# Kernel optimization log

Measured on AMD Instinct MI355X. Metric: run time of the kernel, lower is better.

The kernel has to match this reference:

```python
import jax, jax.numpy as jnp
import numpy as np
from jax import lax

EPS = 1e-5
K = 80000 // 16  # sample_pixels // 16 selected regions per image


def _conv(x, w):
    return lax.conv_general_dilated(x, w, (1, 1), 'VALID',
                                    dimension_numbers=('NHWC', 'HWIO', 'NHWC'))


def _bn(x, g, b, m, v):
    # Keras BatchNormalization in inference mode
    return (x - m) * (g * lax.rsqrt(v + EPS)) + b


def _crop(x, bi, iy, ix, size, pad):
    # tf.image.crop_and_resize with 'nearest' and integer-aligned boxes of span
    # (size+2*pad) reduces to a zero-padded window gather (out-of-bounds -> 0).
    S = size + 2 * pad
    xp = jnp.pad(x, ((0, 0), (pad, pad), (pad, pad), (0, 0)))
    rows = iy[:, None] * size + jnp.arange(S)[None, :]  # padded coords (offset -pad+pad)
    cols = ix[:, None] * size + jnp.arange(S)[None, :]
    return xp[bi[:, None, None], rows[:, :, None], cols[:, None, :], :]  # [N,S,S,C]


def _replace(x, y, bi, iy, ix):
    # scatter 4x4 patches y [N,4,4,C] back into x [B,H,W,C] at block (iy,ix)
    B, H, W, C = x.shape
    x6 = x.reshape(B, H // 4, 4, W // 4, 4, C).transpose(0, 1, 3, 2, 4, 5)
    x6 = x6.at[bi, iy, ix].set(y)
    return x6.transpose(0, 1, 3, 2, 4, 5).reshape(B, H, W, C)


def _forward(src, bgr, pha, fgr, err, hid,
             w1, g1, b1, m1, v1, w2, g2, b2, m2, v2,
             w3, g3, b3, m3, v3, w4, b4):
    B, Hf, Wf = src.shape[:3]
    Hh, Wh, Hq, Wq = Hf // 2, Wf // 2, Hf // 4, Wf // 4
    src_bgr = jnp.concatenate([src, bgr], axis=-1)

    # err already at quarter resolution -> tf bilinear resize is identity
    top_idx = lax.top_k(err[..., 0].reshape(B, -1), K)[1]  # [B,K]
    ref = jnp.zeros((B, Hq * Wq), err.dtype).at[jnp.arange(B)[:, None], top_idx].set(1.0)
    ref = ref.reshape(B, Hq, Wq, 1) * (err > 0).astype(err.dtype)

    bi = jnp.repeat(jnp.arange(B), K)          # [N] patch batch index, N = B*K
    iy = (top_idx // Wq).reshape(-1)
    ix = (top_idx % Wq).reshape(-1)

    x = jnp.concatenate([hid, pha, fgr], axis=-1)  # [B,Hq,Wq,36]
    x = jax.image.resize(x, (B, Hh, Wh, x.shape[-1]), 'bilinear')
    xp = _crop(x, bi, iy, ix, 2, 3)                # [N,8,8,36]
    yh = jax.image.resize(src_bgr, (B, Hh, Wh, 6), 'bilinear')
    yp = _crop(yh, bi, iy, ix, 2, 3)               # [N,8,8,6]

    t = jax.nn.relu(_bn(_conv(jnp.concatenate([xp, yp], -1), w1), g1, b1, m1, v1))  # [N,6,6,24]
    t = jax.nn.relu(_bn(_conv(t, w2), g2, b2, m2, v2))                              # [N,4,4,16]
    t = jax.image.resize(t, (t.shape[0], 8, 8, t.shape[-1]), 'nearest')
    y2 = _crop(src_bgr, bi, iy, ix, 4, 2)                                           # [N,8,8,6]
    t = jax.nn.relu(_bn(_conv(jnp.concatenate([t, y2], -1), w3), g3, b3, m3, v3))   # [N,6,6,12]
    t = _conv(t, w4) + b4                                                            # [N,4,4,4]

    pha_f = jax.image.resize(pha, (B, Hf, Wf, 1), 'bilinear')
    fgr_f = jax.image.resize(fgr, (B, Hf, Wf, 3), 'bilinear')
    pha_f = _replace(pha_f, t[..., :1], bi, iy, ix)
    fgr_f = _replace(fgr_f, t[..., 1:], bi, iy, ix)
    return pha_f, fgr_f, ref


def setup_inputs() -> dict:
    key = jax.random.key(0)
    ks = jax.random.split(key, 10)
    B, H, W = 2, 1088, 1920
    Hq, Wq = H // 4, W // 4
    f = jnp.float32

    def w(k, s):
        return jax.random.normal(k, s, f) * 0.05

    return dict(
        src=jax.random.uniform(ks[0], (B, H, W, 3), f),
        bgr=jax.random.uniform(ks[1], (B, H, W, 3), f),
        pha=jax.random.uniform(ks[2], (B, Hq, Wq, 1), f),
        fgr=jax.random.uniform(ks[3], (B, Hq, Wq, 3), f),
        err=jax.random.uniform(ks[4], (B, Hq, Wq, 1), f),
        hid=jax.random.uniform(ks[5], (B, Hq, Wq, 32), f),
        w1=w(ks[6], (3, 3, 42, 24)),
        g1=jnp.ones((24,), f), b1=jnp.zeros((24,), f), m1=jnp.zeros((24,), f), v1=jnp.ones((24,), f),
        w2=w(ks[7], (3, 3, 24, 16)),
        g2=jnp.ones((16,), f), b2=jnp.zeros((16,), f), m2=jnp.zeros((16,), f), v2=jnp.ones((16,), f),
        w3=w(ks[8], (3, 3, 22, 12)),
        g3=jnp.ones((12,), f), b3=jnp.zeros((12,), f), m3=jnp.zeros((12,), f), v3=jnp.ones((12,), f),
        w4=w(ks[9], (3, 3, 12, 4)), b4=jnp.zeros((4,), f),
    )


def reference(src, bgr, pha, fgr, err, hid,
              w1, g1, b1, m1, v1, w2, g2, b2, m2, v2,
              w3, g3, b3, m3, v3, w4, b4):
    return _forward(src, bgr, pha, fgr, err, hid,
                    w1, g1, b1, m1, v1, w2, g2, b2, m2, v2,
                    w3, g3, b3, m3, v3, w4, b4)
```

## Files before the change

### kernel.cpp

```cpp
#include <hip/hip_runtime.h>

#define EPS 1e-5f

constexpr int NB = 2, HQ = 272, WQ = 480, HH = 544, WH = 960, HF = 1088, WF = 1920;
constexpr int KSEL = 5000;
constexpr int NQ  = HQ * WQ;
constexpr int NEL = NB * NQ;
constexpr int PHA_N = NB * HF * WF;
constexpr int FGR_BASE = PHA_N;
constexpr int REF_BASE = PHA_N * 4;
constexpr int TIE_CAP = 8192;
constexpr int CHUNK = 4080;

constexpr int OFF_H1      = 0;
constexpr int OFF_H2      = 65536;
constexpr int OFF_META    = 327680;
constexpr int OFF_TIECNT  = 327696;
constexpr int OFF_PCOUNT  = 327698;
constexpr int OFF_TIELIST = 327712;
constexpr int OFF_PLIST   = OFF_TIELIST + 2 * TIE_CAP;
constexpr int OFF_WB      = 354112;
constexpr int OFF_YH      = 354176;
constexpr int OFF_WP      = OFF_YH + NB * HH * WH * 6;
constexpr int ZERO_N      = OFF_TIELIST;

typedef short s8v __attribute__((ext_vector_type(8)));
typedef float f4v __attribute__((ext_vector_type(4)));

static __device__ __forceinline__ unsigned short f2bf(float x) {
    unsigned u = __float_as_uint(x);
    u += 0x7fffu + ((u >> 16) & 1u);
    return (unsigned short)(u >> 16);
}
static __device__ __forceinline__ unsigned pack2(float a, float b) {
    return (unsigned)f2bf(a) | ((unsigned)f2bf(b) << 16);
}

__global__ void zero_k(unsigned* __restrict__ p, int n) {
    int i = blockIdx.x * 256 + threadIdx.x;
    if (i < n) p[i] = 0u;
}

__global__ void prepack_all(
    const float* __restrict__ w1, const float* __restrict__ g1, const float* __restrict__ b1,
    const float* __restrict__ m1, const float* __restrict__ v1,
    const float* __restrict__ w2, const float* __restrict__ g2, const float* __restrict__ b2,
    const float* __restrict__ m2, const float* __restrict__ v2,
    const float* __restrict__ w3, const float* __restrict__ g3, const float* __restrict__ b3,
    const float* __restrict__ m3, const float* __restrict__ v3,
    const float* __restrict__ w4, const float* __restrict__ b4,
    unsigned short* __restrict__ P, float* __restrict__ Wb)
{
    int idx = blockIdx.x * 256 + threadIdx.x;
    if (idx < 32256) {
        int j = idx & 7;
        int lane = (idx >> 3) & 63;
        int frag = idx >> 9;
        int li = lane & 15, g = lane >> 4;
        float val = 0.f;
        if (frag < 36) {
            int nt = frag & 1, ks = (frag >> 1) & 1, tap = frag >> 2;
            int n = nt * 16 + li, k = ks * 32 + 8 * g + j;
            if (n < 24 && k < 42) val = w1[(tap * 42 + k) * 24 + n] * (g1[n] / sqrtf(v1[n] + EPS));
        } else if (frag < 45) {
            int tap = frag - 36, k = 8 * g + j;
            if (k < 24) val = w2[(tap * 24 + k) * 16 + li] * (g2[li] / sqrtf(v2[li] + EPS));
        } else if (frag < 54) {
            int tap = frag - 45, k = 8 * g + j;
            if (li < 12 && k < 22) val = w3[(tap * 22 + k) * 12 + li] * (g3[li] / sqrtf(v3[li] + EPS));
        } else {
            int tap = frag - 54, k = 8 * g + j;
            if (li < 4 && k < 12) val = w4[(tap * 12 + k) * 4 + li];
        }
        P[idx] = f2bf(val);
    } else {
        int o = idx - 32256;
        if (o < 24) { float s = g1[o] / sqrtf(v1[o] + EPS); Wb[o] = b1[o] - m1[o] * s; }
        else if (o < 40) { int q = o - 24; float s = g2[q] / sqrtf(v2[q] + EPS); Wb[o] = b2[q] - m2[q] * s; }
        else if (o < 52) { int q = o - 40; float s = g3[q] / sqrtf(v3[q] + EPS); Wb[o] = b3[q] - m3[q] * s; }
        else if (o < 56) Wb[o] = b4[o - 52];
    }
}

__global__ __launch_bounds__(256) void hist_l1(const float* __restrict__ err,
                                               unsigned* __restrict__ hist) {
    __shared__ unsigned lh[16384];
    int b = blockIdx.x >> 5, ch = blockIdx.x & 31;
    for (int i = threadIdx.x; i < 16384; i += 256) lh[i] = 0u;
    __syncthreads();
    int base = b * NQ + ch * CHUNK;
    for (int i = threadIdx.x; i < CHUNK; i += 256) {
        unsigned bin = __float_as_uint(err[base + i]) >> 17;
        atomicAdd(&lh[bin >> 1], 1u << ((bin & 1) * 16));
    }
    __syncthreads();
    unsigned* gh = hist + b * 32768;
    for (int i = threadIdx.x; i < 16384; i += 256) {
        unsigned w = lh[i];
        if (w & 0xFFFFu) atomicAdd(&gh[2 * i], w & 0xFFFFu);
        if (w >> 16)     atomicAdd(&gh[2 * i + 1], w >> 16);
    }
}

__global__ void find_bin(const unsigned* __restrict__ hist, int* __restrict__ meta) {
    int b = blockIdx.x, tid = threadIdx.x;
    const unsigned* h = hist + b * 32768;
    __shared__ unsigned sf[256];
    __shared__ int ssel; __shared__ unsigned scum;
    unsigned own = 0;
    {
        const uint4* hv = (const uint4*)(h + tid * 128);
        for (int i = 0; i < 32; i++) { uint4 v = hv[i]; own += v.x + v.y + v.z + v.w; }
    }
    sf[tid] = own; __syncthreads();
    for (int off = 1; off < 256; off <<= 1) {
        unsigned v = (tid + off < 256) ? sf[tid + off] : 0u;
        __syncthreads(); sf[tid] += v; __syncthreads();
    }
    if (sf[tid] >= (unsigned)KSEL && sf[tid] - own < (unsigned)KSEL) { ssel = tid; scum = sf[tid] - own; }
    __syncthreads();
    int chunk = ssel; unsigned cum = scum;
    unsigned own2 = (tid < 128) ? h[chunk * 128 + tid] : 0u;
    sf[tid] = own2; __syncthreads();
    for (int off = 1; off < 256; off <<= 1) {
        unsigned v = (tid + off < 256) ? sf[tid + off] : 0u;
        __syncthreads(); sf[tid] += v; __syncthreads();
    }
    if (cum + sf[tid] >= (unsigned)KSEL && cum + sf[tid] - own2 < (unsigned)KSEL) {
        meta[b * 8 + 0] = chunk * 128 + tid;
        meta[b * 8 + 1] = (int)(cum + sf[tid] - own2);
    }
}

__global__ void hist_l2(const float* __restrict__ err, const int* __restrict__ meta,
                        unsigned* __restrict__ hist2) {
    int i = blockIdx.x * 256 + threadIdx.x;
    if (i >= NEL) return;
    int b = i / NQ;
    unsigned key = __float_as_uint(err[i]);
    if ((int)(key >> 17) == meta[b * 8 + 0])
        atomicAdd(&hist2[b * 131072 + (key & 0x1FFFFu)], 1u);
}

__global__ void find_thresh(const unsigned* __restrict__ hist2, int* __restrict__ meta) {
    int b = blockIdx.x, tid = threadIdx.x;
    const unsigned* h = hist2 + b * 131072;
    __shared__ unsigned sf[256];
    __shared__ int ssel; __shared__ unsigned scum;
    unsigned own = 0;
    {
        const uint4* hv = (const uint4*)(h + tid * 512);
        for (int i = 0; i < 128; i++) { uint4 v = hv[i]; own += v.x + v.y + v.z + v.w; }
    }
    sf[tid] = own; __syncthreads();
    for (int off = 1; off < 256; off <<= 1) {
        unsigned v = (tid + off < 256) ? sf[tid + off] : 0u;
        __syncthreads(); sf[tid] += v; __syncthreads();
    }
    unsigned cum0 = (unsigned)meta[b * 8 + 1];
    if (cum0 + sf[tid] >= (unsigned)KSEL && cum0 + sf[tid] - own < (unsigned)KSEL) {
        ssel = tid; scum = cum0 + sf[tid] - own;
    }
    __syncthreads();
    int chunk = ssel; unsigned cum = scum;
    unsigned hi = h[chunk * 512 + 2 * tid + 1], lo = h[chunk * 512 + 2 * tid];
    unsigned own2 = hi + lo;
    sf[tid] = own2; __syncthreads();
    for (int off = 1; off < 256; off <<= 1) {
        unsigned v = (tid + off < 256) ? sf[tid + off] : 0u;
        __syncthreads(); sf[tid] += v; __syncthreads();
    }
    if (cum + sf[tid] >= (unsigned)KSEL && cum + sf[tid] - own2 < (unsigned)KSEL) {
        unsigned cumo = cum + sf[tid] - own2;
        int bl; int R;
        if (cumo + hi >= (unsigned)KSEL) { bl = 2 * tid + 1; R = KSEL - (int)cumo; }
        else { bl = 2 * tid; R = KSEL - (int)(cumo + hi); }
        unsigned low17 = (unsigned)(chunk * 512 + bl);
        meta[b * 8 + 2] = (int)(((unsigned)meta[b * 8 + 0] << 17) | low17);
        meta[b * 8 + 3] = R;
    }
}

__global__ void select_tie(const float* __restrict__ err, const int* __restrict__ meta,
                           int* __restrict__ plist, int* __restrict__ pcount,
                           int* __restrict__ tieCnt, int* __restrict__ tieList,
                           float* __restrict__ out) {
    int i = blockIdx.x * 256 + threadIdx.x;
    if (i >= NEL) return;
    int b = i / NQ;
    unsigned key = __float_as_uint(err[i]);
    unsigned T = (unsigned)meta[b * 8 + 2];
    float r = 0.f;
    if (key > T) {
        r = 1.0f;
        int n = atomicAdd(pcount, 1);
        plist[n] = i;
    } else if (key == T) {
        int n = atomicAdd(&tieCnt[b], 1);
        if (n < TIE_CAP) tieList[b * TIE_CAP + n] = i - b * NQ;
    }
    out[REF_BASE + i] = r;
}

__global__ void tie_select(const int* __restrict__ meta, const int* __restrict__ tieCnt,
                           const int* __restrict__ tieList,
                           int* __restrict__ plist, int* __restrict__ pcount,
                           float* __restrict__ out) {
    int b = blockIdx.x;
    int n = tieCnt[b]; if (n > TIE_CAP) n = TIE_CAP;
    int R = meta[b * 8 + 3];
    unsigned T = (unsigned)meta[b * 8 + 2];
    float val = (T > 0u) ? 1.0f : 0.0f;
    for (int e = threadIdx.x; e < n; e += blockDim.x) {
        int my = tieList[b * TIE_CAP + e];
        int rank = 0;
        for (int f = 0; f < n; f++) rank += (tieList[b * TIE_CAP + f] < my) ? 1 : 0;
        if (rank < R) {
            out[REF_BASE + b * NQ + my] = val;
            int q = atomicAdd(pcount, 1);
            plist[q] = b * NQ + my;
        }
    }
}

__global__ void yh_kernel(const float* __restrict__ src, const float* __restrict__ bgr,
                          float* __restrict__ yh) {
    int idx = blockIdx.x * 256 + threadIdx.x;
    if (idx >= NB * HH * WH) return;
    int hx = idx % WH; int t = idx / WH; int hy = t % HH; int b = t / HH;

    float wy[4]; int jy[4]; float sy = 0.f;
#pragma unroll
    for (int k = 0; k < 4; k++) {
        int j = 2 * hy - 1 + k;
        float w = (k == 0 || k == 3) ? 0.125f : 0.375f;
        if (j < 0 || j >= HF) { w = 0.f; j = 0; }
        jy[k] = j; wy[k] = w; sy += w;
    }
    float wx[4]; int jx[4]; float sx = 0.f;
#pragma unroll
    for (int k = 0; k < 4; k++) {
        int j = 2 * hx - 1 + k;
        float w = (k == 0 || k == 3) ? 0.125f : 0.375f;
        if (j < 0 || j >= WF) { w = 0.f; j = 0; }
        jx[k] = j; wx[k] = w; sx += w;
    }
    float inv = 1.f / (sy * sx);
    float acc[6] = {0.f, 0.f, 0.f, 0.f, 0.f, 0.f};
#pragma unroll
    for (int a = 0; a < 4; a++) {
#pragma unroll
        for (int c = 0; c < 4; c++) {
            float w = wy[a] * wx[c];
            int p = ((b * HF + jy[a]) * WF + jx[c]) * 3;
            acc[0] += w * src[p + 0]; acc[1] += w * src[p + 1]; acc[2] += w * src[p + 2];
            acc[3] += w * bgr[p + 0]; acc[4] += w * bgr[p + 1]; acc[5] += w * bgr[p + 2];
        }
    }
    float* Y = yh + (size_t)idx * 6;
#pragma unroll
    for (int j = 0; j < 6; j++) Y[j] = acc[j] * inv;
}

__global__ void base_up(const float* __restrict__ pha, const float* __restrict__ fgr,
                        float* __restrict__ out) {
    int idx = blockIdx.x * 256 + threadIdx.x;
    if (idx >= PHA_N) return;
    int x = idx % WF; int t = idx / WF; int y = t % HF; int b = t / HF;
    int ky = y >> 2, ry = y & 3, kx = x >> 2, rx = x & 3;
    int qy0; float wy0;
    if (ry == 0) { qy0 = ky - 1; wy0 = 0.375f; }
    else if (ry == 1) { qy0 = ky - 1; wy0 = 0.125f; }
    else if (ry == 2) { qy0 = ky; wy0 = 0.875f; }
    else { qy0 = ky; wy0 = 0.625f; }
    int qy1 = qy0 + 1; float wy1 = 1.f - wy0;
    if (qy0 < 0) qy0 = 0; if (qy1 > HQ - 1) qy1 = HQ - 1;
    int qx0; float wx0;
    if (rx == 0) { qx0 = kx - 1; wx0 = 0.375f; }
    else if (rx == 1) { qx0 = kx - 1; wx0 = 0.125f; }
    else if (rx == 2) { qx0 = kx; wx0 = 0.875f; }
    else { qx0 = kx; wx0 = 0.625f; }
    int qx1 = qx0 + 1; float wx1 = 1.f - wx0;
    if (qx0 < 0) qx0 = 0; if (qx1 > WQ - 1) qx1 = WQ - 1;

    int rb = b * HQ;
    int p00 = (rb + qy0) * WQ + qx0, p01 = (rb + qy0) * WQ + qx1;
    int p10 = (rb + qy1) * WQ + qx0, p11 = (rb + qy1) * WQ + qx1;
    float w00 = wy0 * wx0, w01 = wy0 * wx1, w10 = wy1 * wx0, w11 = wy1 * wx1;

    out[idx] = w00 * pha[p00] + w01 * pha[p01] + w10 * pha[p10] + w11 * pha[p11];
    float* fo = out + FGR_BASE + (size_t)idx * 3;
#pragma unroll
    for (int j = 0; j < 3; j++)
        fo[j] = w00 * fgr[p00 * 3 + j] + w01 * fgr[p01 * 3 + j]
              + w10 * fgr[p10 * 3 + j] + w11 * fgr[p11 * 3 + j];
}

__global__ __launch_bounds__(64) void patch_kernel(
    const float* __restrict__ src, const float* __restrict__ bgr,
    const float* __restrict__ pha, const float* __restrict__ fgr,
    const float* __restrict__ hid, const float* __restrict__ yh,
    const float* __restrict__ Wb, const unsigned short* __restrict__ WP,
    const int* __restrict__ plist, const int* __restrict__ pcount,
    float* __restrict__ out)
{
    if ((int)blockIdx.x >= *pcount) return;
    int pk = plist[blockIdx.x];
    int b = pk / NQ, pos = pk % NQ;
    int iy = pos / WQ, ix = pos % WQ;
    int lane = threadIdx.x;
    int g = lane >> 4, li = lane & 15;

    __shared__ __align__(16) unsigned short win[64 * 72];
    __shared__ __align__(16) unsigned short t1s[36 * 40];

    const s8v* WP1v = (const s8v*)WP;
    const s8v* WP2v = WP1v + 36 * 64;
    const s8v* WP3v = WP2v + 9 * 64;
    const s8v* WP4v = WP3v + 9 * 64;

    {
        int r = lane >> 3, c = lane & 7;
        int hy = iy * 2 - 3 + r, hx = ix * 2 - 3 + c;
        unsigned* wrow = (unsigned*)&win[lane * 72];
        if (hy < 0 || hy >= HH || hx < 0 || hx >= WH) {
#pragma unroll
            for (int q = 0; q < 32; q++) wrow[q] = 0u;
        } else {
            int qy0 = (hy - 1) >> 1, qy1 = qy0 + 1;
            float wy0 = (hy & 1) ? 0.75f : 0.25f, wy1 = 1.f - wy0;
            int qx0 = (hx - 1) >> 1, qx1 = qx0 + 1;
            float wx0 = (hx & 1) ? 0.75f : 0.25f, wx1 = 1.f - wx0;
            qy0 = max(qy0, 0); qy1 = min(qy1, HQ - 1);
            qx0 = max(qx0, 0); qx1 = min(qx1, WQ - 1);
            int rb = b * HQ;
            int p00 = (rb + qy0) * WQ + qx0, p01 = (rb + qy0) * WQ + qx1;
            int p10 = (rb + qy1) * WQ + qx0, p11 = (rb + qy1) * WQ + qx1;
            float w00 = wy0 * wx0, w01 = wy0 * wx1, w10 = wy1 * wx0, w11 = wy1 * wx1;
            const float4* h00 = (const float4*)(hid + (size_t)p00 * 32);
            const float4* h01 = (const float4*)(hid + (size_t)p01 * 32);
            const float4* h10 = (const float4*)(hid + (size_t)p10 * 32);
            const float4* h11 = (const float4*)(hid + (size_t)p11 * 32);
#pragma unroll
            for (int q = 0; q < 8; q++) {
                float4 v0 = h00[q], v1 = h01[q], v2 = h10[q], v3 = h11[q];
                float e0 = v0.x * w00 + v1.x * w01 + v2.x * w10 + v3.x * w11;
                float e1 = v0.y * w00 + v1.y * w01 + v2.y * w10 + v3.y * w11;
                float e2 = v0.z * w00 + v1.z * w01 + v2.z * w10 + v3.z * w11;
                float e3 = v0.w * w00 + v1.w * w01 + v2.w * w10 + v3.w * w11;
                wrow[q * 2]     = pack2(e0, e1);
                wrow[q * 2 + 1] = pack2(e2, e3);
            }
            float e32 = pha[p00] * w00 + pha[p01] * w01 + pha[p10] * w10 + pha[p11] * w11;
            float fg[3];
#pragma unroll
            for (int j = 0; j < 3; j++)
                fg[j] = fgr[p00 * 3 + j] * w00 + fgr[p01 * 3 + j] * w01
                      + fgr[p10 * 3 + j] * w10 + fgr[p11 * 3 + j] * w11;
            wrow[16] = pack2(e32, fg[0]);
            wrow[17] = pack2(fg[1], fg[2]);
            const float* Y = yh + (size_t)((b * HH + hy) * WH + hx) * 6;
            wrow[18] = pack2(Y[0], Y[1]);
            wrow[19] = pack2(Y[2], Y[3]);
            wrow[20] = pack2(Y[4], Y[5]);
#pragma unroll
            for (int q = 21; q < 32; q++) wrow[q] = 0u;
        }
    }
    __syncthreads();

    int p0 = li, p1 = 16 + li, p2 = (32 + li > 35) ? 35 : 32 + li;
    int pr0 = (p0 * 171) >> 10, pc0 = p0 - pr0 * 6;
    int pr1 = (p1 * 171) >> 10, pc1 = p1 - pr1 * 6;
    int pr2m = (p2 * 171) >> 10, pc2m = p2 - pr2m * 6;
    int cb0 = pr0 * 8 + pc0, cb1 = pr1 * 8 + pc1, cb2 = pr2m * 8 + pc2m;

    f4v a00 = {0,0,0,0}, a01 = {0,0,0,0}, a10 = {0,0,0,0},
        a11 = {0,0,0,0}, a20 = {0,0,0,0}, a21 = {0,0,0,0};
    {
        const unsigned short* r0 = &win[cb0 * 72 + g * 8];
        const unsigned short* r1 = &win[cb1 * 72 + g * 8];
        const unsigned short* r2 = &win[cb2 * 72 + g * 8];
#pragma unroll
        for (int tap = 0; tap < 9; tap++) {
            const int dr = tap / 3, dc = tap % 3;
            const int coff = (dr * 8 + dc) * 72;
#pragma unroll
            for (int ks = 0; ks < 2; ks++) {
                s8v av0 = *(const s8v*)(r0 + coff + ks * 32);
                s8v av1 = *(const s8v*)(r1 + coff + ks * 32);
                s8v av2 = *(const s8v*)(r2 + coff + ks * 32);
                s8v bv0 = WP1v[((tap * 2 + ks) * 2 + 0) * 64 + lane];
                s8v bv1 = WP1v[((tap * 2 + ks) * 2 + 1) * 64 + lane];
                a00 = __builtin_amdgcn_mfma_f32_16x16x32_bf16(av0, bv0, a00, 0, 0, 0);
                a01 = __builtin_amdgcn_mfma_f32_16x16x32_bf16(av0, bv1, a01, 0, 0, 0);
                a10 = __builtin_amdgcn_mfma_f32_16x16x32_bf16(av1, bv0, a10, 0, 0, 0);
                a11 = __builtin_amdgcn_mfma_f32_16x16x32_bf16(av1, bv1, a11, 0, 0, 0);
                a20 = __builtin_amdgcn_mfma_f32_16x16x32_bf16(av2, bv0, a20, 0, 0, 0);
                a21 = __builtin_amdgcn_mfma_f32_16x16x32_bf16(av2, bv1, a21, 0, 0, 0);
            }
        }
    }
    {
        float b1n0 = Wb[li];
        float b1n1 = (li < 8) ? Wb[16 + li] : 0.f;
#pragma unroll
        for (int r = 0; r < 4; r++) {
            int p = 4 * g + r;
            t1s[p * 40 + li]        = f2bf(fmaxf(a00[r] + b1n0, 0.f));
            t1s[p * 40 + 16 + li]   = f2bf(fmaxf(a01[r] + b1n1, 0.f));
            int pp = 16 + p;
            t1s[pp * 40 + li]       = f2bf(fmaxf(a10[r] + b1n0, 0.f));
            t1s[pp * 40 + 16 + li]  = f2bf(fmaxf(a11[r] + b1n1, 0.f));
            int p2r = 32 + p;
            if (p2r < 36) {
                t1s[p2r * 40 + li]      = f2bf(fmaxf(a20[r] + b1n0, 0.f));
                t1s[p2r * 40 + 16 + li] = f2bf(fmaxf(a21[r] + b1n1, 0.f));
            }
        }
    }
    __syncthreads();

    f4v c2 = {0,0,0,0};
    {
        int pr = li >> 2, pc = li & 3;
#pragma unroll
        for (int tap = 0; tap < 9; tap++) {
            const int dr = tap / 3, dc = tap % 3;
            int cell = (pr + dr) * 6 + pc + dc;
            s8v av = *(const s8v*)&t1s[cell * 40 + g * 8];
            c2 = __builtin_amdgcn_mfma_f32_16x16x32_bf16(av, WP2v[tap * 64 + lane], c2, 0, 0, 0);
        }
    }
    __syncthreads();
    {
        float b2v = Wb[24 + li];
#pragma unroll
        for (int r = 0; r < 4; r++) {
            int p = 4 * g + r;
            unsigned short hv = f2bf(fmaxf(c2[r] + b2v, 0.f));
            int r0 = (p >> 2) * 2, c0 = (p & 3) * 2;
            win[(r0 * 8 + c0) * 40 + li]       = hv;
            win[(r0 * 8 + c0 + 1) * 40 + li]   = hv;
            win[((r0 + 1) * 8 + c0) * 40 + li]     = hv;
            win[((r0 + 1) * 8 + c0 + 1) * 40 + li] = hv;
        }
        int rr = lane >> 3, cc = lane & 7;
        int fy = iy * 4 - 2 + rr, fx = ix * 4 - 2 + cc;
        unsigned* wp3 = (unsigned*)&win[lane * 40];
        if (fy >= 0 && fy < HF && fx >= 0 && fx < WF) {
            const float* sp = src + ((size_t)(b * HF + fy) * WF + fx) * 3;
            const float* bp = bgr + ((size_t)(b * HF + fy) * WF + fx) * 3;
            wp3[8]  = pack2(sp[0], sp[1]);
            wp3[9]  = pack2(sp[2], bp[0]);
            wp3[10] = pack2(bp[1], bp[2]);
        } else {
            wp3[8] = 0u; wp3[9] = 0u; wp3[10] = 0u;
        }
        wp3[11] = 0u; wp3[12] = 0u; wp3[13] = 0u; wp3[14] = 0u; wp3[15] = 0u;
        for (int idx = lane; idx < 36 * 8; idx += 64) {
            int row = idx >> 3;
            ((unsigned*)t1s)[row * 20 + 8 + (idx & 7)] = 0u;
        }
    }
    __syncthreads();

    f4v c30 = {0,0,0,0}, c31 = {0,0,0,0}, c32 = {0,0,0,0};
    {
        const unsigned short* r0 = &win[cb0 * 40 + g * 8];
        const unsigned short* r1 = &win[cb1 * 40 + g * 8];
        const unsigned short* r2 = &win[cb2 * 40 + g * 8];
#pragma unroll
        for (int tap = 0; tap < 9; tap++) {
            const int dr = tap / 3, dc = tap % 3;
            const int coff = (dr * 8 + dc) * 40;
            s8v bv = WP3v[tap * 64 + lane];
            c30 = __builtin_amdgcn_mfma_f32_16x16x32_bf16(*(const s8v*)(r0 + coff), bv, c30, 0, 0, 0);
            c31 = __builtin_amdgcn_mfma_f32_16x16x32_bf16(*(const s8v*)(r1 + coff), bv, c31, 0, 0, 0);
            c32 = __builtin_amdgcn_mfma_f32_16x16x32_bf16(*(const s8v*)(r2 + coff), bv, c32, 0, 0, 0);
        }
    }
    __syncthreads();
    {
        float b3v = (li < 12) ? Wb[40 + li] : 0.f;
#pragma unroll
        for (int r = 0; r < 4; r++) {
            int p = 4 * g + r;
            t1s[p * 40 + li]        = f2bf(fmaxf(c30[r] + b3v, 0.f));
            t1s[(16 + p) * 40 + li] = f2bf(fmaxf(c31[r] + b3v, 0.f));
            int p2r = 32 + p;
            if (p2r < 36) t1s[p2r * 40 + li] = f2bf(fmaxf(c32[r] + b3v, 0.f));
        }
    }
    __syncthreads();

    f4v c4 = {0,0,0,0};
    {
        int pr = li >> 2, pc = li & 3;
#pragma unroll
        for (int tap = 0; tap < 9; tap++) {
            const int dr = tap / 3, dc = tap % 3;
            int cell = (pr + dr) * 6 + pc + dc;
            s8v av = *(const s8v*)&t1s[cell * 40 + g * 8];
            c4 = __builtin_amdgcn_mfma_f32_16x16x32_bf16(av, WP4v[tap * 64 + lane], c4, 0, 0, 0);
        }
    }
    if (li < 4) {
        float b4v = Wb[52 + li];
#pragma unroll
        for (int r = 0; r < 4; r++) {
            int p = 4 * g + r;
            int prow = p >> 2, pcol = p & 3;
            float v = c4[r] + b4v;
            int fidx = (b * HF + iy * 4 + prow) * WF + ix * 4 + pcol;
            if (li == 0) out[fidx] = v;
            else out[FGR_BASE + (size_t)fidx * 3 + (li - 1)] = v;
        }
    }
}

extern "C" void kernel_launch(void* const* d_in, const int* in_sizes, int n_in,
                              void* d_out, int out_size, void* d_ws, size_t ws_size,
                              hipStream_t stream)
{
    const float* src = (const float*)d_in[0];
    const float* bgr = (const float*)d_in[1];
    const float* pha = (const float*)d_in[2];
    const float* fgr = (const float*)d_in[3];
    const float* err = (const float*)d_in[4];
    const float* hid = (const float*)d_in[5];
    const float* w1 = (const float*)d_in[6];
    const float* g1 = (const float*)d_in[7];
    const float* b1 = (const float*)d_in[8];
    const float* m1 = (const float*)d_in[9];
    const float* v1 = (const float*)d_in[10];
    const float* w2 = (const float*)d_in[11];
    const float* g2 = (const float*)d_in[12];
    const float* b2 = (const float*)d_in[13];
    const float* m2 = (const float*)d_in[14];
    const float* v2 = (const float*)d_in[15];
    const float* w3 = (const float*)d_in[16];
    const float* g3 = (const float*)d_in[17];
    const float* b3 = (const float*)d_in[18];
    const float* m3 = (const float*)d_in[19];
    const float* v3 = (const float*)d_in[20];
    const float* w4 = (const float*)d_in[21];
    const float* b4 = (const float*)d_in[22];

    float* out = (float*)d_out;
    unsigned* ws = (unsigned*)d_ws;
    float* wsf = (float*)d_ws;
    int* meta    = (int*)(ws + OFF_META);
    int* tieCnt  = (int*)(ws + OFF_TIECNT);
    int* pcount  = (int*)(ws + OFF_PCOUNT);
    int* tieList = (int*)(ws + OFF_TIELIST);
    int* plist   = (int*)(ws + OFF_PLIST);
    float* Wb = wsf + OFF_WB;
    float* yh = wsf + OFF_YH;
    unsigned short* WP = (unsigned short*)(wsf + OFF_WP);

    zero_k<<<(ZERO_N + 255) / 256, 256, 0, stream>>>(ws, ZERO_N);
    prepack_all<<<127, 256, 0, stream>>>(w1, g1, b1, m1, v1, w2, g2, b2, m2, v2,
                                         w3, g3, b3, m3, v3, w4, b4, WP, Wb);
    hist_l1<<<64, 256, 0, stream>>>(err, ws + OFF_H1);
    find_bin<<<NB, 256, 0, stream>>>(ws + OFF_H1, meta);
    hist_l2<<<(NEL + 255) / 256, 256, 0, stream>>>(err, meta, ws + OFF_H2);
    find_thresh<<<NB, 256, 0, stream>>>(ws + OFF_H2, meta);
    select_tie<<<(NEL + 255) / 256, 256, 0, stream>>>(err, meta, plist, pcount,
                                                      tieCnt, tieList, out);
    tie_select<<<NB, 256, 0, stream>>>(meta, tieCnt, tieList, plist, pcount, out);
    yh_kernel<<<(NB * HH * WH + 255) / 256, 256, 0, stream>>>(src, bgr, yh);
    base_up<<<(PHA_N + 255) / 256, 256, 0, stream>>>(pha, fgr, out);
    patch_kernel<<<NB * KSEL, 64, 0, stream>>>(src, bgr, pha, fgr, hid, yh, Wb, WP,
                                               plist, pcount, out);
}
```

Before: 393.5 us.

## Fuse top-k pipeline into one persistent kernel, vectorize upsample, stage patch inputs

Seven small top-k launches (zero, two histogram passes, threshold finds, select, tie-break) become one 128-block kernel that uses global atomic barriers between phases, removing launch gaps. The full-res bilinear upsample now has each thread produce 4 horizontal outputs, reusing vertical interpolants and writing with float4 stores. The patch kernel stages a 5x5 quarter-res neighbourhood of hid/pha/fgr in shared memory once instead of doing four global gathers per pixel. The software grid barrier depends on all 128 blocks being co-resident and on the magic-word reset logic; if either fails it can deadlock.

```diff
diff --git a/kernel.cpp b/kernel.cpp
--- a/kernel.cpp
+++ b/kernel.cpp
@@ -10,19 +10,23 @@
 constexpr int FGR_BASE = PHA_N;
 constexpr int REF_BASE = PHA_N * 4;
 constexpr int TIE_CAP = 8192;
-constexpr int CHUNK = 4080;
+
+constexpr int TKB = 128;
+constexpr int TKT = TKB * 256;
+constexpr int CH64 = NQ / 64;
+constexpr unsigned SYNC_MAGIC = 0x5A17C0DEu;
 
 constexpr int OFF_H1      = 0;
 constexpr int OFF_H2      = 65536;
 constexpr int OFF_META    = 327680;
 constexpr int OFF_TIECNT  = 327696;
 constexpr int OFF_PCOUNT  = 327698;
+constexpr int OFF_SYNC    = 327700;
 constexpr int OFF_TIELIST = 327712;
 constexpr int OFF_PLIST   = OFF_TIELIST + 2 * TIE_CAP;
 constexpr int OFF_WB      = 354112;
 constexpr int OFF_YH      = 354176;
 constexpr int OFF_WP      = OFF_YH + NB * HH * WH * 6;
-constexpr int ZERO_N      = OFF_TIELIST;
 
 typedef short s8v __attribute__((ext_vector_type(8)));
 typedef float f4v __attribute__((ext_vector_type(4)));
@@ -34,11 +38,6 @@
 }
 static __device__ __forceinline__ unsigned pack2(float a, float b) {
     return (unsigned)f2bf(a) | ((unsigned)f2bf(b) << 16);
-}
-
-__global__ void zero_k(unsigned* __restrict__ p, int n) {
-    int i = blockIdx.x * 256 + threadIdx.x;
-    if (i < n) p[i] = 0u;
 }
 
 __global__ void prepack_all(
@@ -82,143 +81,189 @@
     }
 }
 
-__global__ __launch_bounds__(256) void hist_l1(const float* __restrict__ err,
-                                               unsigned* __restrict__ hist) {
+static __device__ __forceinline__ void gbar(unsigned* sync, int id) {
+    __syncthreads();
+    if (threadIdx.x == 0) {
+        __hip_atomic_fetch_add(&sync[id], 1u, __ATOMIC_ACQ_REL, __HIP_MEMORY_SCOPE_AGENT);
+        while (__hip_atomic_load(&sync[id], __ATOMIC_ACQUIRE, __HIP_MEMORY_SCOPE_AGENT) < (unsigned)TKB)
+            __builtin_amdgcn_s_sleep(2);
+    }
+    __syncthreads();
+}
+
+__global__ __launch_bounds__(256) void topk_all(const float* __restrict__ err,
+                                                unsigned* __restrict__ ws,
+                                                float* __restrict__ out)
+{
+    unsigned* H1 = ws + OFF_H1;
+    unsigned* H2 = ws + OFF_H2;
+    int* meta    = (int*)(ws + OFF_META);
+    int* tieCnt  = (int*)(ws + OFF_TIECNT);
+    int* pcount  = (int*)(ws + OFF_PCOUNT);
+    int* tieList = (int*)(ws + OFF_TIELIST);
+    int* plist   = (int*)(ws + OFF_PLIST);
+    unsigned* sync = ws + OFF_SYNC;
+
     __shared__ unsigned lh[16384];
-    int b = blockIdx.x >> 5, ch = blockIdx.x & 31;
-    for (int i = threadIdx.x; i < 16384; i += 256) lh[i] = 0u;
-    __syncthreads();
-    int base = b * NQ + ch * CHUNK;
-    for (int i = threadIdx.x; i < CHUNK; i += 256) {
-        unsigned bin = __float_as_uint(err[base + i]) >> 17;
-        atomicAdd(&lh[bin >> 1], 1u << ((bin & 1) * 16));
-    }
-    __syncthreads();
-    unsigned* gh = hist + b * 32768;
-    for (int i = threadIdx.x; i < 16384; i += 256) {
-        unsigned w = lh[i];
-        if (w & 0xFFFFu) atomicAdd(&gh[2 * i], w & 0xFFFFu);
-        if (w >> 16)     atomicAdd(&gh[2 * i + 1], w >> 16);
-    }
-}
-
-__global__ void find_bin(const unsigned* __restrict__ hist, int* __restrict__ meta) {
-    int b = blockIdx.x, tid = threadIdx.x;
-    const unsigned* h = hist + b * 32768;
-    __shared__ unsigned sf[256];
     __shared__ int ssel; __shared__ unsigned scum;
-    unsigned own = 0;
-    {
-        const uint4* hv = (const uint4*)(h + tid * 128);
-        for (int i = 0; i < 32; i++) { uint4 v = hv[i]; own += v.x + v.y + v.z + v.w; }
-    }
-    sf[tid] = own; __syncthreads();
-    for (int off = 1; off < 256; off <<= 1) {
-        unsigned v = (tid + off < 256) ? sf[tid + off] : 0u;
-        __syncthreads(); sf[tid] += v; __syncthreads();
-    }
-    if (sf[tid] >= (unsigned)KSEL && sf[tid] - own < (unsigned)KSEL) { ssel = tid; scum = sf[tid] - own; }
-    __syncthreads();
-    int chunk = ssel; unsigned cum = scum;
-    unsigned own2 = (tid < 128) ? h[chunk * 128 + tid] : 0u;
-    sf[tid] = own2; __syncthreads();
-    for (int off = 1; off < 256; off <<= 1) {
-        unsigned v = (tid + off < 256) ? sf[tid + off] : 0u;
-        __syncthreads(); sf[tid] += v; __syncthreads();
-    }
-    if (cum + sf[tid] >= (unsigned)KSEL && cum + sf[tid] - own2 < (unsigned)KSEL) {
-        meta[b * 8 + 0] = chunk * 128 + tid;
-        meta[b * 8 + 1] = (int)(cum + sf[tid] - own2);
-    }
-}
-
-__global__ void hist_l2(const float* __restrict__ err, const int* __restrict__ meta,
-                        unsigned* __restrict__ hist2) {
-    int i = blockIdx.x * 256 + threadIdx.x;
-    if (i >= NEL) return;
-    int b = i / NQ;
-    unsigned key = __float_as_uint(err[i]);
-    if ((int)(key >> 17) == meta[b * 8 + 0])
-        atomicAdd(&hist2[b * 131072 + (key & 0x1FFFFu)], 1u);
-}
-
-__global__ void find_thresh(const unsigned* __restrict__ hist2, int* __restrict__ meta) {
-    int b = blockIdx.x, tid = threadIdx.x;
-    const unsigned* h = hist2 + b * 131072;
-    __shared__ unsigned sf[256];
-    __shared__ int ssel; __shared__ unsigned scum;
-    unsigned own = 0;
-    {
-        const uint4* hv = (const uint4*)(h + tid * 512);
-        for (int i = 0; i < 128; i++) { uint4 v = hv[i]; own += v.x + v.y + v.z + v.w; }
-    }
-    sf[tid] = own; __syncthreads();
-    for (int off = 1; off < 256; off <<= 1) {
-        unsigned v = (tid + off < 256) ? sf[tid + off] : 0u;
-        __syncthreads(); sf[tid] += v; __syncthreads();
-    }
-    unsigned cum0 = (unsigned)meta[b * 8 + 1];
-    if (cum0 + sf[tid] >= (unsigned)KSEL && cum0 + sf[tid] - own < (unsigned)KSEL) {
-        ssel = tid; scum = cum0 + sf[tid] - own;
-    }
-    __syncthreads();
-    int chunk = ssel; unsigned cum = scum;
-    unsigned hi = h[chunk * 512 + 2 * tid + 1], lo = h[chunk * 512 + 2 * tid];
-    unsigned own2 = hi + lo;
-    sf[tid] = own2; __syncthreads();
-    for (int off = 1; off < 256; off <<= 1) {
-        unsigned v = (tid + off < 256) ? sf[tid + off] : 0u;
-        __syncthreads(); sf[tid] += v; __syncthreads();
-    }
-    if (cum + sf[tid] >= (unsigned)KSEL && cum + sf[tid] - own2 < (unsigned)KSEL) {
-        unsigned cumo = cum + sf[tid] - own2;
-        int bl; int R;
-        if (cumo + hi >= (unsigned)KSEL) { bl = 2 * tid + 1; R = KSEL - (int)cumo; }
-        else { bl = 2 * tid; R = KSEL - (int)(cumo + hi); }
-        unsigned low17 = (unsigned)(chunk * 512 + bl);
-        meta[b * 8 + 2] = (int)(((unsigned)meta[b * 8 + 0] << 17) | low17);
-        meta[b * 8 + 3] = R;
-    }
-}
-
-__global__ void select_tie(const float* __restrict__ err, const int* __restrict__ meta,
-                           int* __restrict__ plist, int* __restrict__ pcount,
-                           int* __restrict__ tieCnt, int* __restrict__ tieList,
-                           float* __restrict__ out) {
-    int i = blockIdx.x * 256 + threadIdx.x;
-    if (i >= NEL) return;
-    int b = i / NQ;
-    unsigned key = __float_as_uint(err[i]);
-    unsigned T = (unsigned)meta[b * 8 + 2];
-    float r = 0.f;
-    if (key > T) {
-        r = 1.0f;
-        int n = atomicAdd(pcount, 1);
-        plist[n] = i;
-    } else if (key == T) {
-        int n = atomicAdd(&tieCnt[b], 1);
-        if (n < TIE_CAP) tieList[b * TIE_CAP + n] = i - b * NQ;
-    }
-    out[REF_BASE + i] = r;
-}
-
-__global__ void tie_select(const int* __restrict__ meta, const int* __restrict__ tieCnt,
-                           const int* __restrict__ tieList,
-                           int* __restrict__ plist, int* __restrict__ pcount,
-                           float* __restrict__ out) {
-    int b = blockIdx.x;
-    int n = tieCnt[b]; if (n > TIE_CAP) n = TIE_CAP;
-    int R = meta[b * 8 + 3];
-    unsigned T = (unsigned)meta[b * 8 + 2];
-    float val = (T > 0u) ? 1.0f : 0.0f;
-    for (int e = threadIdx.x; e < n; e += blockDim.x) {
-        int my = tieList[b * TIE_CAP + e];
-        int rank = 0;
-        for (int f = 0; f < n; f++) rank += (tieList[b * TIE_CAP + f] < my) ? 1 : 0;
-        if (rank < R) {
-            out[REF_BASE + b * NQ + my] = val;
-            int q = atomicAdd(pcount, 1);
-            plist[q] = b * NQ + my;
+    int tid = threadIdx.x;
+    int gtid = blockIdx.x * 256 + tid;
+
+    if (blockIdx.x == 0) {
+        if (tid < 8) __hip_atomic_store(&sync[1 + tid], 0u, __ATOMIC_RELAXED, __HIP_MEMORY_SCOPE_AGENT);
+        __syncthreads();
+        if (tid == 0) __hip_atomic_store(&sync[0], SYNC_MAGIC, __ATOMIC_RELEASE, __HIP_MEMORY_SCOPE_AGENT);
+    } else {
+        if (tid == 0)
+            while (__hip_atomic_load(&sync[0], __ATOMIC_ACQUIRE, __HIP_MEMORY_SCOPE_AGENT) != SYNC_MAGIC)
+                __builtin_amdgcn_s_sleep(2);
+        __syncthreads();
+    }
+
+    {
+        uint4 z; z.x = z.y = z.z = z.w = 0u;
+        uint4* p4 = (uint4*)ws;
+        for (int i = gtid; i < 81920; i += TKT) p4[i] = z;
+        if (gtid < 19) ws[OFF_META + gtid] = 0u;
+    }
+    gbar(sync, 1);
+
+    {
+        int b = blockIdx.x >> 6, ch = blockIdx.x & 63;
+        for (int i = tid; i < 16384; i += 256) lh[i] = 0u;
+        __syncthreads();
+        int base = b * NQ + ch * CH64;
+        for (int i = tid; i < CH64; i += 256) {
+            unsigned bin = __float_as_uint(err[base + i]) >> 17;
+            atomicAdd(&lh[bin >> 1], 1u << ((bin & 1) * 16));
+        }
+        __syncthreads();
+        unsigned* gh = H1 + b * 32768;
+        for (int i = tid; i < 16384; i += 256) {
+            unsigned w = lh[i];
+            if (w & 0xFFFFu) atomicAdd(&gh[2 * i], w & 0xFFFFu);
+            if (w >> 16)     atomicAdd(&gh[2 * i + 1], w >> 16);
+        }
+    }
+    gbar(sync, 2);
+
+    if (blockIdx.x < NB) {
+        int b = blockIdx.x;
+        const unsigned* h = H1 + b * 32768;
+        unsigned* sf = lh;
+        unsigned own = 0;
+        {
+            const uint4* hv = (const uint4*)(h + tid * 128);
+            for (int i = 0; i < 32; i++) { uint4 v = hv[i]; own += v.x + v.y + v.z + v.w; }
+        }
+        sf[tid] = own; __syncthreads();
+        for (int off = 1; off < 256; off <<= 1) {
+            unsigned v = (tid + off < 256) ? sf[tid + off] : 0u;
+            __syncthreads(); sf[tid] += v; __syncthreads();
+        }
+        if (sf[tid] >= (unsigned)KSEL && sf[tid] - own < (unsigned)KSEL) { ssel = tid; scum = sf[tid] - own; }
+        __syncthreads();
+        int chunk = ssel; unsigned cum = scum;
+        unsigned own2 = (tid < 128) ? h[chunk * 128 + tid] : 0u;
+        __syncthreads();
+        sf[tid] = own2; __syncthreads();
+        for (int off = 1; off < 256; off <<= 1) {
+            unsigned v = (tid + off < 256) ? sf[tid + off] : 0u;
+            __syncthreads(); sf[tid] += v; __syncthreads();
+        }
+        if (cum + sf[tid] >= (unsigned)KSEL && cum + sf[tid] - own2 < (unsigned)KSEL) {
+            meta[b * 8 + 0] = chunk * 128 + tid;
+            meta[b * 8 + 1] = (int)(cum + sf[tid] - own2);
+        }
+    }
+    gbar(sync, 3);
+
+    {
+        int m0 = meta[0], m1 = meta[8];
+        for (int i = gtid; i < NEL; i += TKT) {
+            int b = (i >= NQ) ? 1 : 0;
+            unsigned key = __float_as_uint(err[i]);
+            if ((int)(key >> 17) == (b ? m1 : m0))
+                atomicAdd(&H2[b * 131072 + (key & 0x1FFFFu)], 1u);
+        }
+    }
+    gbar(sync, 4);
+
+    if (blockIdx.x < NB) {
+        int b = blockIdx.x;
+        const unsigned* h = H2 + b * 131072;
+        unsigned* sf = lh;
+        unsigned own = 0;
+        {
+            const uint4* hv = (const uint4*)(h + tid * 512);
+            for (int i = 0; i < 128; i++) { uint4 v = hv[i]; own += v.x + v.y + v.z + v.w; }
+        }
+        sf[tid] = own; __syncthreads();
+        for (int off = 1; off < 256; off <<= 1) {
+            unsigned v = (tid + off < 256) ? sf[tid + off] : 0u;
+            __syncthreads(); sf[tid] += v; __syncthreads();
+        }
+        unsigned cum0 = (unsigned)meta[b * 8 + 1];
+        if (cum0 + sf[tid] >= (unsigned)KSEL && cum0 + sf[tid] - own < (unsigned)KSEL) {
+            ssel = tid; scum = cum0 + sf[tid] - own;
+        }
+        __syncthreads();
+        int chunk = ssel; unsigned cum = scum;
+        unsigned hi = h[chunk * 512 + 2 * tid + 1], lo = h[chunk * 512 + 2 * tid];
+        unsigned own2 = hi + lo;
+        __syncthreads();
+        sf[tid] = own2; __syncthreads();
+        for (int off = 1; off < 256; off <<= 1) {
+            unsigned v = (tid + off < 256) ? sf[tid + off] : 0u;
+            __syncthreads(); sf[tid] += v; __syncthreads();
+        }
+        if (cum + sf[tid] >= (unsigned)KSEL && cum + sf[tid] - own2 < (unsigned)KSEL) {
+            unsigned cumo = cum + sf[tid] - own2;
+            int bl; int R;
+            if (cumo + hi >= (unsigned)KSEL) { bl = 2 * tid + 1; R = KSEL - (int)cumo; }
+            else { bl = 2 * tid; R = KSEL - (int)(cumo + hi); }
+            unsigned low17 = (unsigned)(chunk * 512 + bl);
+            meta[b * 8 + 2] = (int)(((unsigned)meta[b * 8 + 0] << 17) | low17);
+            meta[b * 8 + 3] = R;
+        }
+    }
+    gbar(sync, 5);
+
+    {
+        unsigned T0 = (unsigned)meta[2], T1 = (unsigned)meta[10];
+        for (int i = gtid; i < NEL; i += TKT) {
+            int b = (i >= NQ) ? 1 : 0;
+            unsigned key = __float_as_uint(err[i]);
+            unsigned T = b ? T1 : T0;
+            float r = 0.f;
+            if (key > T) {
+                r = 1.0f;
+                int n = atomicAdd(pcount, 1);
+                plist[n] = i;
+            } else if (key == T) {
+                int n = atomicAdd(&tieCnt[b], 1);
+                if (n < TIE_CAP) tieList[b * TIE_CAP + n] = i - b * NQ;
+            }
+            out[REF_BASE + i] = r;
+        }
+    }
+    gbar(sync, 6);
+
+    if (blockIdx.x < NB) {
+        int b = blockIdx.x;
+        int n = tieCnt[b]; if (n > TIE_CAP) n = TIE_CAP;
+        int R = meta[b * 8 + 3];
+        unsigned T = (unsigned)meta[b * 8 + 2];
+        float val = (T > 0u) ? 1.0f : 0.0f;
+        for (int e = tid; e < n; e += 256) {
+            int my = tieList[b * TIE_CAP + e];
+            int rank = 0;
+            for (int f = 0; f < n; f++) rank += (tieList[b * TIE_CAP + f] < my) ? 1 : 0;
+            if (rank < R) {
+                out[REF_BASE + b * NQ + my] = val;
+                int q = atomicAdd(pcount, 1);
+                plist[q] = b * NQ + my;
+            }
         }
     }
 }
@@ -262,12 +307,15 @@
     for (int j = 0; j < 6; j++) Y[j] = acc[j] * inv;
 }
 
-__global__ void base_up(const float* __restrict__ pha, const float* __restrict__ fgr,
-                        float* __restrict__ out) {
-    int idx = blockIdx.x * 256 + threadIdx.x;
-    if (idx >= PHA_N) return;
-    int x = idx % WF; int t = idx / WF; int y = t % HF; int b = t / HF;
-    int ky = y >> 2, ry = y & 3, kx = x >> 2, rx = x & 3;
+__global__ __launch_bounds__(256) void base_up4(const float* __restrict__ pha,
+                                                const float* __restrict__ fgr,
+                                                float* __restrict__ out) {
+    int t = blockIdx.x * 256 + threadIdx.x;
+    int kx = t % 480;
+    int rest = t / 480;
+    int y = rest % HF; int b = rest / HF;
+
+    int ky = y >> 2, ry = y & 3;
     int qy0; float wy0;
     if (ry == 0) { qy0 = ky - 1; wy0 = 0.375f; }
     else if (ry == 1) { qy0 = ky - 1; wy0 = 0.125f; }
@@ -275,25 +323,38 @@
     else { qy0 = ky; wy0 = 0.625f; }
     int qy1 = qy0 + 1; float wy1 = 1.f - wy0;
     if (qy0 < 0) qy0 = 0; if (qy1 > HQ - 1) qy1 = HQ - 1;
-    int qx0; float wx0;
-    if (rx == 0) { qx0 = kx - 1; wx0 = 0.375f; }
-    else if (rx == 1) { qx0 = kx - 1; wx0 = 0.125f; }
-    else if (rx == 2) { qx0 = kx; wx0 = 0.875f; }
-    else { qx0 = kx; wx0 = 0.625f; }
-    int qx1 = qx0 + 1; float wx1 = 1.f - wx0;
-    if (qx0 < 0) qx0 = 0; if (qx1 > WQ - 1) qx1 = WQ - 1;
-
-    int rb = b * HQ;
-    int p00 = (rb + qy0) * WQ + qx0, p01 = (rb + qy0) * WQ + qx1;
-    int p10 = (rb + qy1) * WQ + qx0, p11 = (rb + qy1) * WQ + qx1;
-    float w00 = wy0 * wx0, w01 = wy0 * wx1, w10 = wy1 * wx0, w11 = wy1 * wx1;
-
-    out[idx] = w00 * pha[p00] + w01 * pha[p01] + w10 * pha[p10] + w11 * pha[p11];
-    float* fo = out + FGR_BASE + (size_t)idx * 3;
-#pragma unroll
-    for (int j = 0; j < 3; j++)
-        fo[j] = w00 * fgr[p00 * 3 + j] + w01 * fgr[p01 * 3 + j]
-              + w10 * fgr[p10 * 3 + j] + w11 * fgr[p11 * 3 + j];
+
+    int c0 = max(kx - 1, 0), c2 = min(kx + 1, WQ - 1);
+    int r0 = (b * HQ + qy0) * WQ, r1 = (b * HQ + qy1) * WQ;
+
+    float A = wy0 * pha[r0 + c0] + wy1 * pha[r1 + c0];
+    float B = wy0 * pha[r0 + kx] + wy1 * pha[r1 + kx];
+    float C = wy0 * pha[r0 + c2] + wy1 * pha[r1 + c2];
+    float4 po;
+    po.x = 0.375f * A + 0.625f * B;
+    po.y = 0.125f * A + 0.875f * B;
+    po.z = 0.875f * B + 0.125f * C;
+    po.w = 0.625f * B + 0.375f * C;
+    int oidx = (b * HF + y) * WF + kx * 4;
+    *(float4*)(out + oidx) = po;
+
+    float f[12];
+#pragma unroll
+    for (int j = 0; j < 3; j++) {
+        float a = wy0 * fgr[(r0 + c0) * 3 + j] + wy1 * fgr[(r1 + c0) * 3 + j];
+        float bb = wy0 * fgr[(r0 + kx) * 3 + j] + wy1 * fgr[(r1 + kx) * 3 + j];
+        float c = wy0 * fgr[(r0 + c2) * 3 + j] + wy1 * fgr[(r1 + c2) * 3 + j];
+        f[0 + j] = 0.375f * a + 0.625f * bb;
+        f[3 + j] = 0.125f * a + 0.875f * bb;
+        f[6 + j] = 0.875f * bb + 0.125f * c;
+        f[9 + j] = 0.625f * bb + 0.375f * c;
+    }
+    float* fo = out + FGR_BASE + (size_t)oidx * 3;
+    float4 s0, s1, s2;
+    s0.x = f[0]; s0.y = f[1]; s0.z = f[2];  s0.w = f[3];
+    s1.x = f[4]; s1.y = f[5]; s1.z = f[6];  s1.w = f[7];
+    s2.x = f[8]; s2.y = f[9]; s2.z = f[10]; s2.w = f[11];
+    *(float4*)(fo + 0) = s0; *(float4*)(fo + 4) = s1; *(float4*)(fo + 8) = s2;
 }
 
 __global__ __launch_bounds__(64) void patch_kernel(
@@ -312,7 +373,9 @@
     int g = lane >> 4, li = lane & 15;
 
     __shared__ __align__(16) unsigned short win[64 * 72];
-    __shared__ __align__(16) unsigned short t1s[36 * 40];
+    __shared__ __align__(16) float uu[900];
+    unsigned short* t1s = (unsigned short*)uu;
+    float* qs = uu;
 
     const s8v* WP1v = (const s8v*)WP;
     const s8v* WP2v = WP1v + 36 * 64;
@@ -320,6 +383,27 @@
     const s8v* WP4v = WP3v + 9 * 64;
 
     {
+        for (int t = lane; t < 200; t += 64) {
+            int px = t >> 3, q = t & 7;
+            int jy = px / 5, jx = px - jy * 5;
+            int ry = min(max(iy - 2 + jy, 0), HQ - 1);
+            int rx = min(max(ix - 2 + jx, 0), WQ - 1);
+            float4 v = ((const float4*)(hid + ((size_t)((b * HQ + ry) * WQ + rx)) * 32))[q];
+            float* d = qs + px * 36 + q * 4;
+            d[0] = v.x; d[1] = v.y; d[2] = v.z; d[3] = v.w;
+        }
+        for (int t = lane; t < 100; t += 64) {
+            int px = t >> 2, c = t & 3;
+            int jy = px / 5, jx = px - jy * 5;
+            int ry = min(max(iy - 2 + jy, 0), HQ - 1);
+            int rx = min(max(ix - 2 + jx, 0), WQ - 1);
+            int base = (b * HQ + ry) * WQ + rx;
+            qs[px * 36 + 32 + c] = (c == 0) ? pha[base] : fgr[base * 3 + (c - 1)];
+        }
+    }
+    __syncthreads();
+
+    {
         int r = lane >> 3, c = lane & 7;
         int hy = iy * 2 - 3 + r, hx = ix * 2 - 3 + c;
         unsigned* wrow = (unsigned*)&win[lane * 72];
@@ -327,38 +411,30 @@
 #pragma unroll
             for (int q = 0; q < 32; q++) wrow[q] = 0u;
         } else {
-            int qy0 = (hy - 1) >> 1, qy1 = qy0 + 1;
+            int ay = ((r - 4) >> 1) + 2;
+            int ax = ((c - 4) >> 1) + 2;
             float wy0 = (hy & 1) ? 0.75f : 0.25f, wy1 = 1.f - wy0;
-            int qx0 = (hx - 1) >> 1, qx1 = qx0 + 1;
             float wx0 = (hx & 1) ? 0.75f : 0.25f, wx1 = 1.f - wx0;
-            qy0 = max(qy0, 0); qy1 = min(qy1, HQ - 1);
-            qx0 = max(qx0, 0); qx1 = min(qx1, WQ - 1);
-            int rb = b * HQ;
-            int p00 = (rb + qy0) * WQ + qx0, p01 = (rb + qy0) * WQ + qx1;
-            int p10 = (rb + qy1) * WQ + qx0, p11 = (rb + qy1) * WQ + qx1;
             float w00 = wy0 * wx0, w01 = wy0 * wx1, w10 = wy1 * wx0, w11 = wy1 * wx1;
-            const float4* h00 = (const float4*)(hid + (size_t)p00 * 32);
-            const float4* h01 = (const float4*)(hid + (size_t)p01 * 32);
-            const float4* h10 = (const float4*)(hid + (size_t)p10 * 32);
-            const float4* h11 = (const float4*)(hid + (size_t)p11 * 32);
+            const float* q00 = qs + (ay * 5 + ax) * 36;
+            const float* q01 = q00 + 36;
+            const float* q10 = q00 + 180;
+            const float* q11 = q10 + 36;
 #pragma unroll
             for (int q = 0; q < 8; q++) {
-                float4 v0 = h00[q], v1 = h01[q], v2 = h10[q], v3 = h11[q];
-                float e0 = v0.x * w00 + v1.x * w01 + v2.x * w10 + v3.x * w11;
-                float e1 = v0.y * w00 + v1.y * w01 + v2.y * w10 + v3.y * w11;
-                float e2 = v0.z * w00 + v1.z * w01 + v2.z * w10 + v3.z * w11;
-                float e3 = v0.w * w00 + v1.w * w01 + v2.w * w10 + v3.w * w11;
+                float e0 = q00[q*4+0]*w00 + q01[q*4+0]*w01 + q10[q*4+0]*w10 + q11[q*4+0]*w11;
+                float e1 = q00[q*4+1]*w00 + q01[q*4+1]*w01 + q10[q*4+1]*w10 + q11[q*4+1]*w11;
+                float e2 = q00[q*4+2]*w00 + q01[q*4+2]*w01 + q10[q*4+2]*w10 + q11[q*4+2]*w11;
+                float e3 = q00[q*4+3]*w00 + q01[q*4+3]*w01 + q10[q*4+3]*w10 + q11[q*4+3]*w11;
                 wrow[q * 2]     = pack2(e0, e1);
                 wrow[q * 2 + 1] = pack2(e2, e3);
             }
-            float e32 = pha[p00] * w00 + pha[p01] * w01 + pha[p10] * w10 + pha[p11] * w11;
-            float fg[3];
-#pragma unroll
-            for (int j = 0; j < 3; j++)
-                fg[j] = fgr[p00 * 3 + j] * w00 + fgr[p01 * 3 + j] * w01
-                      + fgr[p10 * 3 + j] * w10 + fgr[p11 * 3 + j] * w11;
-            wrow[16] = pack2(e32, fg[0]);
-            wrow[17] = pack2(fg[1], fg[2]);
+            float e32 = q00[32]*w00 + q01[32]*w01 + q10[32]*w10 + q11[32]*w11;
+            float f0  = q00[33]*w00 + q01[33]*w01 + q10[33]*w10 + q11[33]*w11;
+            float f1  = q00[34]*w00 + q01[34]*w01 + q10[34]*w10 + q11[34]*w11;
+            float f2  = q00[35]*w00 + q01[35]*w01 + q10[35]*w10 + q11[35]*w11;
+            wrow[16] = pack2(e32, f0);
+            wrow[17] = pack2(f1, f2);
             const float* Y = yh + (size_t)((b * HH + hy) * WH + hx) * 6;
             wrow[18] = pack2(Y[0], Y[1]);
             wrow[19] = pack2(Y[2], Y[3]);
@@ -440,8 +516,8 @@
             int p = 4 * g + r;
             unsigned short hv = f2bf(fmaxf(c2[r] + b2v, 0.f));
             int r0 = (p >> 2) * 2, c0 = (p & 3) * 2;
-            win[(r0 * 8 + c0) * 40 + li]       = hv;
-            win[(r0 * 8 + c0 + 1) * 40 + li]   = hv;
+            win[(r0 * 8 + c0) * 40 + li]           = hv;
+            win[(r0 * 8 + c0 + 1) * 40 + li]       = hv;
             win[((r0 + 1) * 8 + c0) * 40 + li]     = hv;
             win[((r0 + 1) * 8 + c0 + 1) * 40 + li] = hv;
         }
@@ -550,27 +626,17 @@
     float* out = (float*)d_out;
     unsigned* ws = (unsigned*)d_ws;
     float* wsf = (float*)d_ws;
-    int* meta    = (int*)(ws + OFF_META);
-    int* tieCnt  = (int*)(ws + OFF_TIECNT);
+    int* plist   = (int*)(ws + OFF_PLIST);
     int* pcount  = (int*)(ws + OFF_PCOUNT);
-    int* tieList = (int*)(ws + OFF_TIELIST);
-    int* plist   = (int*)(ws + OFF_PLIST);
     float* Wb = wsf + OFF_WB;
     float* yh = wsf + OFF_YH;
     unsigned short* WP = (unsigned short*)(wsf + OFF_WP);
 
-    zero_k<<<(ZERO_N + 255) / 256, 256, 0, stream>>>(ws, ZERO_N);
     prepack_all<<<127, 256, 0, stream>>>(w1, g1, b1, m1, v1, w2, g2, b2, m2, v2,
                                          w3, g3, b3, m3, v3, w4, b4, WP, Wb);
-    hist_l1<<<64, 256, 0, stream>>>(err, ws + OFF_H1);
-    find_bin<<<NB, 256, 0, stream>>>(ws + OFF_H1, meta);
-    hist_l2<<<(NEL + 255) / 256, 256, 0, stream>>>(err, meta, ws + OFF_H2);
-    find_thresh<<<NB, 256, 0, stream>>>(ws + OFF_H2, meta);
-    select_tie<<<(NEL + 255) / 256, 256, 0, stream>>>(err, meta, plist, pcount,
-                                                      tieCnt, tieList, out);
-    tie_select<<<NB, 256, 0, stream>>>(meta, tieCnt, tieList, plist, pcount, out);
+    topk_all<<<TKB, 256, 0, stream>>>(err, ws, out);
     yh_kernel<<<(NB * HH * WH + 255) / 256, 256, 0, stream>>>(src, bgr, yh);
-    base_up<<<(PHA_N + 255) / 256, 256, 0, stream>>>(pha, fgr, out);
+    base_up4<<<PHA_N / 4 / 256, 256, 0, stream>>>(pha, fgr, out);
     patch_kernel<<<NB * KSEL, 64, 0, stream>>>(src, bgr, pha, fgr, hid, yh, Wb, WP,
                                                plist, pcount, out);
 }
```

Result: slower. 432.8 us (+10.0%).
